# Optimization experiments

Measured on AMD Instinct MI355X. Metric: run time of the kernel, lower is better.

## Reference

```python
import jax, jax.numpy as jnp
import numpy as np

EPS = 1e-5
DN = ('NCHW', 'OIHW', 'NCHW')


def ternarize(w):
    """Ternary Weight Network quantization with straight-through estimator.
    delta = 0.7 * mean|w|; alpha = mean of |w| over kept entries.
    """
    aw = jnp.abs(w)
    delta = 0.7 * aw.mean()
    mask = (aw > delta).astype(w.dtype)
    alpha = (aw * mask).sum() / jnp.maximum(mask.sum(), 1.0)
    q = alpha * jnp.sign(w) * mask
    return w + jax.lax.stop_gradient(q - w)


def bn(y, g, b, m, v):
    scale = (g / jnp.sqrt(v + EPS))[None, :, None, None]
    shift = (b - m * g / jnp.sqrt(v + EPS))[None, :, None, None]
    return y * scale + shift


def relu6(y):
    return jnp.clip(y, 0.0, 6.0)


def conv(x, w, stride=1, padding='VALID'):
    return jax.lax.conv_general_dilated(
        x, w, window_strides=(stride, stride), padding=padding,
        dimension_numbers=DN)


def setup_inputs() -> dict:
    key = jax.random.key(0)
    ks = jax.random.split(key, 16)
    inp, oup, expand = 32, 32, 6
    hidden = inp * expand  # 192
    B, H, W = 16, 112, 112
    d = {}
    d['x'] = jax.random.normal(ks[0], (B, inp, H, W), dtype=jnp.float32)
    # 1x1 expand conv
    d['w1'] = jax.random.normal(ks[1], (hidden, inp, 1, 1), dtype=jnp.float32) * 0.1
    d['g1'] = 1.0 + 0.1 * jax.random.normal(ks[2], (hidden,), dtype=jnp.float32)
    d['b1'] = 0.1 * jax.random.normal(ks[3], (hidden,), dtype=jnp.float32)
    d['m1'] = 0.1 * jax.random.normal(ks[4], (hidden,), dtype=jnp.float32)
    d['v1'] = jax.random.uniform(ks[5], (hidden,), minval=0.5, maxval=1.5, dtype=jnp.float32)
    # 3x3 dense conv (no groups in the source -> dense, not depthwise)
    d['w2'] = jax.random.normal(ks[6], (hidden, hidden, 3, 3), dtype=jnp.float32) * 0.05
    d['g2'] = 1.0 + 0.1 * jax.random.normal(ks[7], (hidden,), dtype=jnp.float32)
    d['b2'] = 0.1 * jax.random.normal(ks[8], (hidden,), dtype=jnp.float32)
    d['m2'] = 0.1 * jax.random.normal(ks[9], (hidden,), dtype=jnp.float32)
    d['v2'] = jax.random.uniform(ks[10], (hidden,), minval=0.5, maxval=1.5, dtype=jnp.float32)
    # 1x1 project conv
    d['w3'] = jax.random.normal(ks[11], (oup, hidden, 1, 1), dtype=jnp.float32) * 0.1
    d['g3'] = 1.0 + 0.1 * jax.random.normal(ks[12], (oup,), dtype=jnp.float32)
    d['b3'] = 0.1 * jax.random.normal(ks[13], (oup,), dtype=jnp.float32)
    d['m3'] = 0.1 * jax.random.normal(ks[14], (oup,), dtype=jnp.float32)
    d['v3'] = jax.random.uniform(ks[15], (oup,), minval=0.5, maxval=1.5, dtype=jnp.float32)
    return d


def reference(x, w1, g1, b1, m1, v1, w2, g2, b2, m2, v2, w3, g3, b3, m3, v3):
    # expand: 1x1 ternary conv -> BN -> ReLU6
    h = relu6(bn(conv(x, ternarize(w1)), g1, b1, m1, v1))
    # 3x3 ternary conv (stride=1, padding=1) -> BN -> ReLU6
    h = relu6(bn(conv(h, ternarize(w2), stride=1, padding=((1, 1), (1, 1))), g2, b2, m2, v2))
    # project: 1x1 ternary conv -> BN (no activation)
    h = bn(conv(h, ternarize(w3)), g3, b3, m3, v3)
    # residual connection (stride==1 and inp==oup)
    return x + h
```

## Files before the change

kernel.cpp:

```cpp
#include <hip/hip_runtime.h>


typedef __bf16 bf16x8 __attribute__((ext_vector_type(8)));
typedef __bf16 bf16x4 __attribute__((ext_vector_type(4)));
typedef float  f32x4  __attribute__((ext_vector_type(4)));

#define EPSBN 1e-5f

__device__ __forceinline__ void glds16(const void* g, void* l) {
  __builtin_amdgcn_global_load_lds(
      (const __attribute__((address_space(1))) void*)g,
      (__attribute__((address_space(3))) void*)l, 16, 0, 0);
}

__device__ __forceinline__ __bf16 tern(float w, float delta) {
  float aw = fabsf(w);
  float q = (aw > delta) ? ((w > 0.0f) ? 1.0f : -1.0f) : 0.0f;
  return (__bf16)q;
}


__global__ void stats_pass1(const float* __restrict__ w1, const float* __restrict__ w2,
                            const float* __restrict__ w3, double* __restrict__ pa) {
  __shared__ double red[256];
  int b = blockIdx.x, tid = threadIdx.x;
  int tix = b >> 5, slice = b & 31;
  const float* w = (tix == 0) ? w1 : (tix == 1) ? w2 : w3;
  int len = (tix == 1) ? 331776 : 6144;
  int per = len >> 5;
  int start = slice * per, end = start + per;
  double s = 0.0;
  for (int i = start + tid; i < end; i += 256) s += (double)fabsf(w[i]);
  red[tid] = s; __syncthreads();
  for (int off = 128; off > 0; off >>= 1) {
    if (tid < off) red[tid] += red[tid + off];
    __syncthreads();
  }
  if (tid == 0) pa[b] = red[0];
}

__global__ void stats_pass2(const float* __restrict__ w1, const float* __restrict__ w2,
                            const float* __restrict__ w3, const double* __restrict__ pa,
                            double* __restrict__ ps2, double* __restrict__ pc2) {
  __shared__ double red[256];
  int b = blockIdx.x, tid = threadIdx.x;
  int tix = b >> 5, slice = b & 31;
  const float* w = (tix == 0) ? w1 : (tix == 1) ? w2 : w3;
  int len = (tix == 1) ? 331776 : 6144;
  double tot = 0.0;
  for (int k = 0; k < 32; ++k) tot += pa[tix * 32 + k];
  float delta = 0.7f * (float)(tot / (double)len);
  int per = len >> 5;
  int start = slice * per, end = start + per;
  double s2 = 0.0, c2 = 0.0;
  for (int i = start + tid; i < end; i += 256) {
    float aw = fabsf(w[i]);
    if (aw > delta) { s2 += (double)aw; c2 += 1.0; }
  }
  red[tid] = s2; __syncthreads();
  for (int off = 128; off > 0; off >>= 1) {
    if (tid < off) red[tid] += red[tid + off];
    __syncthreads();
  }
  if (tid == 0) ps2[b] = red[0];
  __syncthreads();
  red[tid] = c2; __syncthreads();
  for (int off = 128; off > 0; off >>= 1) {
    if (tid < off) red[tid] += red[tid + off];
    __syncthreads();
  }
  if (tid == 0) pc2[b] = red[0];
}

__global__ void stats_pass3(const double* __restrict__ pa, const double* __restrict__ ps2,
                            const double* __restrict__ pc2, float* __restrict__ stats) {
  int tix = blockIdx.x;
  if (threadIdx.x != 0) return;
  double tot = 0.0, s2 = 0.0, c2 = 0.0;
  for (int k = 0; k < 32; ++k) {
    tot += pa[tix * 32 + k];
    s2  += ps2[tix * 32 + k];
    c2  += pc2[tix * 32 + k];
  }
  int len = (tix == 1) ? 331776 : 6144;
  stats[tix * 2]     = 0.7f * (float)(tot / (double)len);
  stats[tix * 2 + 1] = (float)(s2 / fmax(c2, 1.0));
}

__global__ void pack_kernel(
    const float* __restrict__ w1, const float* __restrict__ w2, const float* __restrict__ w3,
    const float* __restrict__ g1, const float* __restrict__ b1, const float* __restrict__ m1, const float* __restrict__ v1,
    const float* __restrict__ g2, const float* __restrict__ b2, const float* __restrict__ m2, const float* __restrict__ v2,
    const float* __restrict__ g3, const float* __restrict__ b3, const float* __restrict__ m3, const float* __restrict__ v3,
    const float* __restrict__ stats,
    __bf16* __restrict__ w1p, __bf16* __restrict__ w2p, __bf16* __restrict__ w3p,
    float* __restrict__ sc1, float* __restrict__ sh1,
    float* __restrict__ sc2, float* __restrict__ sh2,
    float* __restrict__ sc3, float* __restrict__ sh3) {
  int idx = blockIdx.x * 256 + threadIdx.x;
  if (idx < 331776) {
    float delta2 = stats[2];
    int c = idx / 6144, rem = idx - c * 6144;
    int co = rem >> 5, r5 = rem & 31;
    int cp = r5 >> 3, lo = r5 & 7;
    int tap = c / 6, cb = c - tap * 6;
    int ci = ((cp ^ ((co >> 2) & 3)) << 3) | lo;
    int cifull = cb * 32 + ci;
    w2p[idx] = tern(w2[(co * 192 + cifull) * 9 + tap], delta2);
    return;
  }
  idx -= 331776;
  if (idx < 6144) {
    int co = idx >> 5, c = (idx >> 3) & 3, lo = idx & 7;
    int ci = ((c ^ ((co >> 2) & 3)) << 3) | lo;
    w1p[idx] = tern(w1[co * 32 + ci], stats[0]);
    return;
  }
  idx -= 6144;
  if (idx < 6144) {
    int kc = idx >> 11, rem = idx & 2047;
    int co = rem >> 6, c = (rem >> 3) & 7, lo = rem & 7;
    int ci = ((c ^ (co & 7)) << 3) | lo;
    w3p[idx] = tern(w3[co * 192 + kc * 64 + ci], stats[4]);
    return;
  }
  idx -= 6144;
  if (idx < 192) {
    float rs = rsqrtf(v1[idx] + EPSBN);
    sc1[idx] = g1[idx] * rs * stats[1];
    sh1[idx] = b1[idx] - m1[idx] * g1[idx] * rs;
    return;
  }
  idx -= 192;
  if (idx < 192) {
    float rs = rsqrtf(v2[idx] + EPSBN);
    sc2[idx] = g2[idx] * rs * stats[3];
    sh2[idx] = b2[idx] - m2[idx] * g2[idx] * rs;
    return;
  }
  idx -= 192;
  if (idx < 32) {
    float rs = rsqrtf(v3[idx] + EPSBN);
    sc3[idx] = g3[idx] * rs * stats[5];
    sh3[idx] = b3[idx] - m3[idx] * g3[idx] * rs;
  }
}

__global__ __launch_bounds__(256)
void conv1_kernel(const float* __restrict__ x, const __bf16* __restrict__ w1p,
                  const float* __restrict__ scale1, const float* __restrict__ shift1,
                  __bf16* __restrict__ h1p) {
  __shared__ __bf16 smA[112 * 32];
  __shared__ __bf16 smB[192 * 32];
  int tid = threadIdx.x, lane = tid & 63, wave = tid >> 6;
  int h = blockIdx.x, n = blockIdx.y;

  for (int t = wave; t < 12; t += 4)
    glds16((const char*)w1p + t * 1024 + lane * 16, (char*)smB + t * 1024);

  const float* xrow = x + (long)n * 401408 + h * 112;
  for (int i = 0; i < 14; ++i) {
    int f = i * 256 + tid;
    int ci = f / 112, w = f - ci * 112;
    int col = ((ci >> 3) ^ ((w >> 2) & 3));
    smA[w * 32 + (col << 3) + (ci & 7)] = (__bf16)xrow[ci * 12544 + w];
  }
  __syncthreads();

  int mrow = lane & 15, quad = lane >> 4;
  int col16 = (quad ^ ((mrow >> 2) & 3)) * 16;
  int c0 = wave * 48;

  bf16x8 aw[3], bv[7];
#pragma unroll
  for (int ic = 0; ic < 3; ++ic)
    aw[ic] = *(const bf16x8*)((const char*)smB + (c0 + ic * 16 + mrow) * 64 + col16);
#pragma unroll
  for (int jp = 0; jp < 7; ++jp)
    bv[jp] = *(const bf16x8*)((const char*)smA + (jp * 16 + mrow) * 64 + col16);

  f32x4 acc[7][3];
#pragma unroll
  for (int jp = 0; jp < 7; ++jp)
#pragma unroll
    for (int ic = 0; ic < 3; ++ic) acc[jp][ic] = (f32x4)0.0f;

#pragma unroll
  for (int jp = 0; jp < 7; ++jp)
#pragma unroll
    for (int ic = 0; ic < 3; ++ic)
      acc[jp][ic] = __builtin_amdgcn_mfma_f32_16x16x32_bf16(aw[ic], bv[jp], acc[jp][ic], 0, 0, 0);

  __bf16* obase = h1p + ((long)(n * 114 + h + 1) * 114 + 1) * 192;
#pragma unroll
  for (int ic = 0; ic < 3; ++ic) {
    int co0 = c0 + ic * 16 + quad * 4;
    float4 sc = *(const float4*)(scale1 + co0);
    float4 sh = *(const float4*)(shift1 + co0);
#pragma unroll
    for (int jp = 0; jp < 7; ++jp) {
      int w = jp * 16 + mrow;
      bf16x4 o;
      o[0] = (__bf16)fminf(fmaxf(acc[jp][ic][0] * sc.x + sh.x, 0.0f), 6.0f);
      o[1] = (__bf16)fminf(fmaxf(acc[jp][ic][1] * sc.y + sh.y, 0.0f), 6.0f);
      o[2] = (__bf16)fminf(fmaxf(acc[jp][ic][2] * sc.z + sh.z, 0.0f), 6.0f);
      o[3] = (__bf16)fminf(fmaxf(acc[jp][ic][3] * sc.w + sh.w, 0.0f), 6.0f);
      *(bf16x4*)(obase + w * 192 + co0) = o;
    }
  }

  float4 z = make_float4(0.f, 0.f, 0.f, 0.f);
  if (tid < 48) {
    int px = (tid < 24) ? 0 : 113;
    int c8 = (tid < 24) ? tid : tid - 24;
    *(float4*)((char*)h1p + ((long)((n * 114 + h + 1) * 114 + px) * 384) + c8 * 16) = z;
  }
  if (h == 0) {
    for (int c = tid; c < 2736; c += 256)
      *(float4*)((char*)h1p + (long)(n * 114) * 114 * 384 + c * 16) = z;
  }
  if (h == 111) {
    for (int c = tid; c < 2736; c += 256)
      *(float4*)((char*)h1p + (long)(n * 114 + 113) * 114 * 384 + c * 16) = z;
  }
}

__global__ __launch_bounds__(256, 2)
void conv2_kernel(const __bf16* __restrict__ h1p, const __bf16* __restrict__ w2p,
                  const float* __restrict__ scale2, const float* __restrict__ shift2,
                  __bf16* __restrict__ h2) {
  __shared__ __bf16 smA[456 * 32];
  __shared__ __bf16 smB[2 * 192 * 32];
  int tid = threadIdx.x, lane = tid & 63, wave = tid >> 6;
  int bh = blockIdx.x, n = blockIdx.y;
  int h0 = bh * 2;

  int aoff[8];
#pragma unroll
  for (int it = 0; it < 8; ++it) {
    int t = wave + it * 4;
    int s = t * 64 + lane;
    if (s < 1824) {
      int q = s >> 2, c = s & 3;
      int q_log = c ^ ((q >> 2) & 3);
      int prow = q / 114, pcol = q - prow * 114;
      aoff[it] = ((n * 114 + h0 + prow) * 114 + pcol) * 384 + q_log * 16;
    } else {
      aoff[it] = -1;
    }
  }

  int pg = wave >> 1, cg = wave & 1;
  int mrow = lane & 15, quad = lane >> 4;
  int col16 = (quad ^ ((mrow >> 2) & 3)) * 16;
  const char* h1b = (const char*)h1p;
  const char* w2b = (const char*)w2p;

  f32x4 acc[7][6];
#pragma unroll
  for (int jp = 0; jp < 7; ++jp)
#pragma unroll
    for (int ic = 0; ic < 6; ++ic) acc[jp][ic] = (f32x4)0.0f;

  for (int cb = 0; cb < 6; ++cb) {
#pragma unroll
    for (int it = 0; it < 8; ++it) {
      int t = wave + it * 4;
      if (aoff[it] >= 0)
        glds16(h1b + aoff[it] + cb * 64, (char*)smA + t * 1024);
    }
#pragma unroll
    for (int it = 0; it < 3; ++it) {
      int t = wave + it * 4;
      glds16(w2b + (long)cb * 12288 + t * 1024 + lane * 16, (char*)smB + t * 1024);
    }
    __syncthreads();

    for (int tap = 0; tap < 9; ++tap) {
      int cur = tap & 1;
      if (tap < 8) {
#pragma unroll
        for (int it = 0; it < 3; ++it) {
          int t = wave + it * 4;
          glds16(w2b + (long)((tap + 1) * 6 + cb) * 12288 + t * 1024 + lane * 16,
                 (char*)smB + (cur ^ 1) * 12288 + t * 1024);
        }
      }
      int dy = tap / 3, dx = tap - dy * 3;
      const char* bbuf = (const char*)smB + cur * 12288;
      bf16x8 aw[6];
#pragma unroll
      for (int ic = 0; ic < 6; ++ic)
        aw[ic] = *(const bf16x8*)(bbuf + (cg * 96 + ic * 16 + mrow) * 64 + col16);
      int base = (pg + dy) * 114 + dx;
#pragma unroll
      for (int jp = 0; jp < 7; ++jp) {
        int row = base + jp * 16 + mrow;
        bf16x8 av = *(const bf16x8*)((const char*)smA + row * 64 +
                                     ((quad ^ ((row >> 2) & 3)) * 16));
#pragma unroll
        for (int ic = 0; ic < 6; ++ic)
          acc[jp][ic] = __builtin_amdgcn_mfma_f32_16x16x32_bf16(aw[ic], av, acc[jp][ic], 0, 0, 0);
      }
      __syncthreads();
    }
  }

  int h = h0 + pg;
  __bf16* orow = h2 + (long)((n * 112 + h) * 112) * 192;
#pragma unroll
  for (int ic = 0; ic < 6; ++ic) {
    int co0 = cg * 96 + ic * 16 + quad * 4;
    float4 sc = *(const float4*)(scale2 + co0);
    float4 sh = *(const float4*)(shift2 + co0);
#pragma unroll
    for (int jp = 0; jp < 7; ++jp) {
      int w = jp * 16 + mrow;
      bf16x4 o;
      o[0] = (__bf16)fminf(fmaxf(acc[jp][ic][0] * sc.x + sh.x, 0.0f), 6.0f);
      o[1] = (__bf16)fminf(fmaxf(acc[jp][ic][1] * sc.y + sh.y, 0.0f), 6.0f);
      o[2] = (__bf16)fminf(fmaxf(acc[jp][ic][2] * sc.z + sh.z, 0.0f), 6.0f);
      o[3] = (__bf16)fminf(fmaxf(acc[jp][ic][3] * sc.w + sh.w, 0.0f), 6.0f);
      *(bf16x4*)(orow + w * 192 + co0) = o;
    }
  }
}

__global__ __launch_bounds__(128)
void conv3_kernel(const __bf16* __restrict__ h2, const __bf16* __restrict__ w3p,
                  const float* __restrict__ scale3, const float* __restrict__ shift3,
                  const float* __restrict__ x, float* __restrict__ out) {
  __shared__ __bf16 smA[112 * 64];
  __shared__ __bf16 smB[32 * 64];
  int tid = threadIdx.x, lane = tid & 63, wv = tid >> 6;
  int h = blockIdx.x, n = blockIdx.y;
  int mrow = lane & 15, quad = lane >> 4;
  int swz7 = mrow & 7;

  const char* h2b = (const char*)h2 + (long)((n * 112 + h) * 112) * 384;
  f32x4 acc[7];
#pragma unroll
  for (int i = 0; i < 7; ++i) acc[i] = (f32x4)0.0f;

  for (int kc = 0; kc < 3; ++kc) {
    for (int t = wv; t < 18; t += 2) {
      if (t < 14) {
        int slot = t * 64 + lane;
        int w = slot >> 3, s = slot & 7;
        glds16(h2b + w * 384 + kc * 128 + (s ^ (w & 7)) * 16, (char*)smA + t * 1024);
      } else {
        glds16((const char*)w3p + kc * 4096 + (t - 14) * 1024 + lane * 16,
               (char*)smB + (t - 14) * 1024);
      }
    }
    __syncthreads();
    bf16x8 a[7][2], b[2];
#pragma unroll
    for (int ks = 0; ks < 2; ++ks) {
      int col = ((ks * 4 + quad) ^ swz7) * 16;
      b[ks] = *(const bf16x8*)((const char*)smB + (wv * 16 + mrow) * 128 + col);
#pragma unroll
      for (int i = 0; i < 7; ++i)
        a[i][ks] = *(const bf16x8*)((const char*)smA + (i * 16 + mrow) * 128 + col);
    }
    __syncthreads();
#pragma unroll
    for (int ks = 0; ks < 2; ++ks)
#pragma unroll
      for (int i = 0; i < 7; ++i)
        acc[i] = __builtin_amdgcn_mfma_f32_16x16x32_bf16(a[i][ks], b[ks], acc[i], 0, 0, 0);
  }

  int co = wv * 16 + mrow;
  float sc = scale3[co], sh = shift3[co];
  long obase = ((long)(n * 32 + co) * 112 + h) * 112;
  const float* xb = x + obase;
  float* ob = out + obase;
#pragma unroll
  for (int i = 0; i < 7; ++i) {
    int w0 = i * 16 + quad * 4;
    float4 xv = *(const float4*)(xb + w0);
    float4 o;
    o.x = acc[i][0] * sc + sh + xv.x;
    o.y = acc[i][1] * sc + sh + xv.y;
    o.z = acc[i][2] * sc + sh + xv.z;
    o.w = acc[i][3] * sc + sh + xv.w;
    *(float4*)(ob + w0) = o;
  }
}

extern "C" void kernel_launch(void* const* d_in, const int* in_sizes, int n_in,
                              void* d_out, int out_size, void* d_ws, size_t ws_size,
                              hipStream_t stream) {
  const float* x  = (const float*)d_in[0];
  const float* w1 = (const float*)d_in[1];
  const float* g1 = (const float*)d_in[2];
  const float* b1 = (const float*)d_in[3];
  const float* m1 = (const float*)d_in[4];
  const float* v1 = (const float*)d_in[5];
  const float* w2 = (const float*)d_in[6];
  const float* g2 = (const float*)d_in[7];
  const float* b2 = (const float*)d_in[8];
  const float* m2 = (const float*)d_in[9];
  const float* v2 = (const float*)d_in[10];
  const float* w3 = (const float*)d_in[11];
  const float* g3 = (const float*)d_in[12];
  const float* b3 = (const float*)d_in[13];
  const float* m3 = (const float*)d_in[14];
  const float* v3 = (const float*)d_in[15];
  float* out = (float*)d_out;

  char* ws = (char*)d_ws;
  float*  stats = (float*)ws;
  double* pa    = (double*)(ws + 256);
  double* ps2   = (double*)(ws + 1024);
  double* pc2   = (double*)(ws + 1792);
  float* sc1 = (float*)(ws + 2560);
  float* sh1 = (float*)(ws + 3328);
  float* sc2 = (float*)(ws + 4096);
  float* sh2 = (float*)(ws + 4864);
  float* sc3 = (float*)(ws + 5632);
  float* sh3 = (float*)(ws + 5760);
  __bf16* w1p = (__bf16*)(ws + 8192);
  __bf16* w3p = (__bf16*)(ws + 20480);
  __bf16* w2p = (__bf16*)(ws + 32768);
  __bf16* h1p = (__bf16*)(ws + (1 << 20));
  __bf16* h2  = (__bf16*)(ws + (1 << 20) + 79847424);

  hipLaunchKernelGGL(stats_pass1, dim3(96), dim3(256), 0, stream, w1, w2, w3, pa);
  hipLaunchKernelGGL(stats_pass2, dim3(96), dim3(256), 0, stream, w1, w2, w3, pa, ps2, pc2);
  hipLaunchKernelGGL(stats_pass3, dim3(3), dim3(64), 0, stream, pa, ps2, pc2, stats);
  hipLaunchKernelGGL(pack_kernel, dim3(1346), dim3(256), 0, stream, w1, w2, w3,
                     g1, b1, m1, v1, g2, b2, m2, v2, g3, b3, m3, v3, stats,
                     w1p, w2p, w3p, sc1, sh1, sc2, sh2, sc3, sh3);
  hipLaunchKernelGGL(conv1_kernel, dim3(112, 16), dim3(256), 0, stream, x, w1p, sc1, sh1, h1p);
  hipLaunchKernelGGL(conv2_kernel, dim3(56, 16), dim3(256), 0, stream, h1p, w2p, sc2, sh2, h2);
  hipLaunchKernelGGL(conv3_kernel, dim3(112, 16), dim3(128), 0, stream, h2, w3p, sc3, sh3, x, out);
}
```

Before: 300.6 us.

## Restructure conv kernels: register-load conv1 input, one-row conv2 blocks, swizzled h2

conv1 now loads x straight into MFMA B-fragment registers and no longer stages it in shared memory. conv2 is retiled to one output row per 128-thread block (2 waves, each covering 96 channels), so the halo stage is 3 input rows instead of 4. conv2 also writes h2 with an XOR-swizzled channel layout. conv3 then loads the whole 192-channel row and all weights in one async pass, with a single barrier instead of per-chunk syncs. The risks are more redundant halo reads per output row in conv2, fewer waves per block, and uncoalesced strided global loads of x in conv1.

```diff
diff --git a/kernel.cpp b/kernel.cpp
--- a/kernel.cpp
+++ b/kernel.cpp
@@ -150,7 +150,6 @@
 void conv1_kernel(const float* __restrict__ x, const __bf16* __restrict__ w1p,
                   const float* __restrict__ scale1, const float* __restrict__ shift1,
                   __bf16* __restrict__ h1p) {
-  __shared__ __bf16 smA[112 * 32];
   __shared__ __bf16 smB[192 * 32];
   int tid = threadIdx.x, lane = tid & 63, wave = tid >> 6;
   int h = blockIdx.x, n = blockIdx.y;
@@ -158,26 +157,24 @@
   for (int t = wave; t < 12; t += 4)
     glds16((const char*)w1p + t * 1024 + lane * 16, (char*)smB + t * 1024);
 
+  int mrow = lane & 15, quad = lane >> 4;
   const float* xrow = x + (long)n * 401408 + h * 112;
-  for (int i = 0; i < 14; ++i) {
-    int f = i * 256 + tid;
-    int ci = f / 112, w = f - ci * 112;
-    int col = ((ci >> 3) ^ ((w >> 2) & 3));
-    smA[w * 32 + (col << 3) + (ci & 7)] = (__bf16)xrow[ci * 12544 + w];
+
+  bf16x8 bv[7];
+#pragma unroll
+  for (int jp = 0; jp < 7; ++jp) {
+#pragma unroll
+    for (int r = 0; r < 8; ++r)
+      bv[jp][r] = (__bf16)xrow[(quad * 8 + r) * 12544 + jp * 16 + mrow];
   }
   __syncthreads();
 
-  int mrow = lane & 15, quad = lane >> 4;
   int col16 = (quad ^ ((mrow >> 2) & 3)) * 16;
   int c0 = wave * 48;
-
-  bf16x8 aw[3], bv[7];
+  bf16x8 aw[3];
 #pragma unroll
   for (int ic = 0; ic < 3; ++ic)
     aw[ic] = *(const bf16x8*)((const char*)smB + (c0 + ic * 16 + mrow) * 64 + col16);
-#pragma unroll
-  for (int jp = 0; jp < 7; ++jp)
-    bv[jp] = *(const bf16x8*)((const char*)smA + (jp * 16 + mrow) * 64 + col16);
 
   f32x4 acc[7][3];
 #pragma unroll
@@ -225,22 +222,21 @@
   }
 }
 
-__global__ __launch_bounds__(256, 2)
+__global__ __launch_bounds__(128)
 void conv2_kernel(const __bf16* __restrict__ h1p, const __bf16* __restrict__ w2p,
                   const float* __restrict__ scale2, const float* __restrict__ shift2,
                   __bf16* __restrict__ h2) {
-  __shared__ __bf16 smA[456 * 32];
+  __shared__ __bf16 smA[342 * 32];
   __shared__ __bf16 smB[2 * 192 * 32];
   int tid = threadIdx.x, lane = tid & 63, wave = tid >> 6;
-  int bh = blockIdx.x, n = blockIdx.y;
-  int h0 = bh * 2;
-
-  int aoff[8];
-#pragma unroll
-  for (int it = 0; it < 8; ++it) {
-    int t = wave + it * 4;
+  int h0 = blockIdx.x, n = blockIdx.y;
+
+  int aoff[11];
+#pragma unroll
+  for (int it = 0; it < 11; ++it) {
+    int t = it * 2 + wave;
     int s = t * 64 + lane;
-    if (s < 1824) {
+    if (s < 1368) {
       int q = s >> 2, c = s & 3;
       int q_log = c ^ ((q >> 2) & 3);
       int prow = q / 114, pcol = q - prow * 114;
@@ -250,7 +246,7 @@
     }
   }
 
-  int pg = wave >> 1, cg = wave & 1;
+  int cg = wave;
   int mrow = lane & 15, quad = lane >> 4;
   int col16 = (quad ^ ((mrow >> 2) & 3)) * 16;
   const char* h1b = (const char*)h1p;
@@ -264,14 +260,14 @@
 
   for (int cb = 0; cb < 6; ++cb) {
 #pragma unroll
-    for (int it = 0; it < 8; ++it) {
-      int t = wave + it * 4;
+    for (int it = 0; it < 11; ++it) {
+      int t = it * 2 + wave;
       if (aoff[it] >= 0)
         glds16(h1b + aoff[it] + cb * 64, (char*)smA + t * 1024);
     }
 #pragma unroll
-    for (int it = 0; it < 3; ++it) {
-      int t = wave + it * 4;
+    for (int it = 0; it < 6; ++it) {
+      int t = it * 2 + wave;
       glds16(w2b + (long)cb * 12288 + t * 1024 + lane * 16, (char*)smB + t * 1024);
     }
     __syncthreads();
@@ -280,8 +276,8 @@
       int cur = tap & 1;
       if (tap < 8) {
 #pragma unroll
-        for (int it = 0; it < 3; ++it) {
-          int t = wave + it * 4;
+        for (int it = 0; it < 6; ++it) {
+          int t = it * 2 + wave;
           glds16(w2b + (long)((tap + 1) * 6 + cb) * 12288 + t * 1024 + lane * 16,
                  (char*)smB + (cur ^ 1) * 12288 + t * 1024);
         }
@@ -292,7 +288,7 @@
 #pragma unroll
       for (int ic = 0; ic < 6; ++ic)
         aw[ic] = *(const bf16x8*)(bbuf + (cg * 96 + ic * 16 + mrow) * 64 + col16);
-      int base = (pg + dy) * 114 + dx;
+      int base = dy * 114 + dx;
 #pragma unroll
       for (int jp = 0; jp < 7; ++jp) {
         int row = base + jp * 16 + mrow;
@@ -306,8 +302,7 @@
     }
   }
 
-  int h = h0 + pg;
-  __bf16* orow = h2 + (long)((n * 112 + h) * 112) * 192;
+  long pixbase = (long)((n * 112 + h0) * 112);
 #pragma unroll
   for (int ic = 0; ic < 6; ++ic) {
     int co0 = cg * 96 + ic * 16 + quad * 4;
@@ -321,7 +316,8 @@
       o[1] = (__bf16)fminf(fmaxf(acc[jp][ic][1] * sc.y + sh.y, 0.0f), 6.0f);
       o[2] = (__bf16)fminf(fmaxf(acc[jp][ic][2] * sc.z + sh.z, 0.0f), 6.0f);
       o[3] = (__bf16)fminf(fmaxf(acc[jp][ic][3] * sc.w + sh.w, 0.0f), 6.0f);
-      *(bf16x4*)(orow + w * 192 + co0) = o;
+      long baddr = (pixbase + w) * 384 + (((co0 >> 3) ^ (w & 7)) << 4) + (co0 & 7) * 2;
+      *(bf16x4*)((char*)h2 + baddr) = o;
     }
   }
 }
@@ -330,48 +326,46 @@
 void conv3_kernel(const __bf16* __restrict__ h2, const __bf16* __restrict__ w3p,
                   const float* __restrict__ scale3, const float* __restrict__ shift3,
                   const float* __restrict__ x, float* __restrict__ out) {
-  __shared__ __bf16 smA[112 * 64];
-  __shared__ __bf16 smB[32 * 64];
+  __shared__ __bf16 smA[112 * 192];
+  __shared__ __bf16 smB[3 * 32 * 64];
   int tid = threadIdx.x, lane = tid & 63, wv = tid >> 6;
   int h = blockIdx.x, n = blockIdx.y;
   int mrow = lane & 15, quad = lane >> 4;
-  int swz7 = mrow & 7;
 
   const char* h2b = (const char*)h2 + (long)((n * 112 + h) * 112) * 384;
+#pragma unroll
+  for (int it = 0; it < 21; ++it) {
+    int t = it * 2 + wv;
+    glds16(h2b + t * 1024 + lane * 16, (char*)smA + t * 1024);
+  }
+#pragma unroll
+  for (int it = 0; it < 6; ++it) {
+    int t = it * 2 + wv;
+    glds16((const char*)w3p + t * 1024 + lane * 16, (char*)smB + t * 1024);
+  }
+  __syncthreads();
+
+  int co = wv * 16 + mrow;
   f32x4 acc[7];
 #pragma unroll
   for (int i = 0; i < 7; ++i) acc[i] = (f32x4)0.0f;
 
+#pragma unroll
   for (int kc = 0; kc < 3; ++kc) {
-    for (int t = wv; t < 18; t += 2) {
-      if (t < 14) {
-        int slot = t * 64 + lane;
-        int w = slot >> 3, s = slot & 7;
-        glds16(h2b + w * 384 + kc * 128 + (s ^ (w & 7)) * 16, (char*)smA + t * 1024);
-      } else {
-        glds16((const char*)w3p + kc * 4096 + (t - 14) * 1024 + lane * 16,
-               (char*)smB + (t - 14) * 1024);
+#pragma unroll
+    for (int ks = 0; ks < 2; ++ks) {
+      bf16x8 b = *(const bf16x8*)((const char*)smB + kc * 4096 + co * 128 +
+                                  (((ks * 4 + quad) ^ (co & 7)) << 4));
+#pragma unroll
+      for (int i = 0; i < 7; ++i) {
+        int w = i * 16 + mrow;
+        bf16x8 a = *(const bf16x8*)((const char*)smA + w * 384 + kc * 128 +
+                                    (((ks * 4 + quad) ^ (w & 7)) << 4));
+        acc[i] = __builtin_amdgcn_mfma_f32_16x16x32_bf16(a, b, acc[i], 0, 0, 0);
       }
     }
-    __syncthreads();
-    bf16x8 a[7][2], b[2];
-#pragma unroll
-    for (int ks = 0; ks < 2; ++ks) {
-      int col = ((ks * 4 + quad) ^ swz7) * 16;
-      b[ks] = *(const bf16x8*)((const char*)smB + (wv * 16 + mrow) * 128 + col);
-#pragma unroll
-      for (int i = 0; i < 7; ++i)
-        a[i][ks] = *(const bf16x8*)((const char*)smA + (i * 16 + mrow) * 128 + col);
-    }
-    __syncthreads();
-#pragma unroll
-    for (int ks = 0; ks < 2; ++ks)
-#pragma unroll
-      for (int i = 0; i < 7; ++i)
-        acc[i] = __builtin_amdgcn_mfma_f32_16x16x32_bf16(a[i][ks], b[ks], acc[i], 0, 0, 0);
-  }
-
-  int co = wv * 16 + mrow;
+  }
+
   float sc = scale3[co], sh = shift3[co];
   long obase = ((long)(n * 32 + co) * 112 + h) * 112;
   const float* xb = x + obase;
@@ -434,6 +428,6 @@
                      g1, b1, m1, v1, g2, b2, m2, v2, g3, b3, m3, v3, stats,
                      w1p, w2p, w3p, sc1, sh1, sc2, sh2, sc3, sh3);
   hipLaunchKernelGGL(conv1_kernel, dim3(112, 16), dim3(256), 0, stream, x, w1p, sc1, sh1, h1p);
-  hipLaunchKernelGGL(conv2_kernel, dim3(56, 16), dim3(256), 0, stream, h1p, w2p, sc2, sh2, h2);
+  hipLaunchKernelGGL(conv2_kernel, dim3(112, 16), dim3(128), 0, stream, h1p, w2p, sc2, sh2, h2);
   hipLaunchKernelGGL(conv3_kernel, dim3(112, 16), dim3(128), 0, stream, h2, w3p, sc3, sh3, x, out);
 }
```

Result: slower. 406.5 us (+35.2%).
